# Optimization experiments

Measured on AMD Instinct MI355X. Metric: run time of the kernel, lower is better.

The kernel has to match this reference:

```python
import jax, jax.numpy as jnp
import numpy as np

B, T, D, H = 8, 1024, 512, 8
D4 = 4 * D
SIGMA = 16.0
EPS = 1e-5


def layer_norm(x, w, b):
    m = jnp.mean(x, axis=-1, keepdims=True)
    v = jnp.mean((x - m) ** 2, axis=-1, keepdims=True)
    return (x - m) * jax.lax.rsqrt(v + EPS) * w + b


def setup_inputs() -> dict:
    key = jax.random.key(0)
    ks = jax.random.split(key, 12)
    return {
        "x": jax.random.normal(ks[0], (B, T, D), jnp.float32),
        "posv": jax.random.randint(ks[1], (B, T), 0, 64, jnp.int32),
        "posh": jax.random.randint(ks[2], (B, T), 0, 64, jnp.int32),
        "norm1_w": jnp.ones((D,), jnp.float32),
        "norm1_b": jnp.zeros((D,), jnp.float32),
        "in_w": jax.random.normal(ks[3], (3 * D, D), jnp.float32) * (D ** -0.5),
        "in_b": jnp.zeros((3 * D,), jnp.float32),
        "out_w": jax.random.normal(ks[4], (D, D), jnp.float32) * (D ** -0.5),
        "out_b": jnp.zeros((D,), jnp.float32),
        "norm2_w": jnp.ones((D,), jnp.float32),
        "norm2_b": jnp.zeros((D,), jnp.float32),
        "w1": jax.random.normal(ks[5], (D4, D), jnp.float32) * (D ** -0.5),
        "b1": jnp.zeros((D4,), jnp.float32),
        "w2": jax.random.normal(ks[6], (D, D4), jnp.float32) * (D4 ** -0.5),
        "b2": jnp.zeros((D,), jnp.float32),
        "gate": jnp.array(0.0, jnp.float32),
    }


def reference(x, posv, posh, norm1_w, norm1_b, in_w, in_b, out_w, out_b,
              norm2_w, norm2_b, w1, b1, w2, b2, gate):
    hd = D // H
    residual = x
    xn = layer_norm(x, norm1_w, norm1_b)

    # --- standard multi-head self-attention (dropout=eval identity) ---
    qkv = xn @ in_w.T + in_b                       # [B,T,3D]
    q, k, v = jnp.split(qkv, 3, axis=-1)
    q = q.reshape(B, T, H, hd).transpose(0, 2, 1, 3)  # [B,H,T,hd]
    k = k.reshape(B, T, H, hd).transpose(0, 2, 1, 3)
    v = v.reshape(B, T, H, hd).transpose(0, 2, 1, 3)
    scores = jnp.einsum("bhqd,bhkd->bhqk", q, k) * (hd ** -0.5)
    attn = jax.nn.softmax(scores, axis=-1)
    ctx = jnp.einsum("bhqk,bhkd->bhqd", attn, v)   # [B,H,T,hd]
    ctx = ctx.transpose(0, 2, 1, 3).reshape(B, T, D)
    std_out = ctx @ out_w.T + out_b

    # --- Gaussian kernel position attention ---
    pos = jnp.stack([posv, posh], axis=-1).astype(jnp.float32)  # [B,T,2]
    dist_sq = jnp.sum((pos[:, :, None, :] - pos[:, None, :, :]) ** 2, axis=-1)  # [B,T,T]
    kw = jnp.exp(-dist_sq / (2.0 * SIGMA ** 2))
    kw = kw / jnp.sum(kw, axis=-1, keepdims=True)
    kernel_out = kw @ xn                            # [B,T,D]

    g = jax.nn.sigmoid(gate)
    x1 = residual + g * std_out + (1.0 - g) * kernel_out

    # --- MLP block ---
    xn2 = layer_norm(x1, norm2_w, norm2_b)
    h = jax.nn.gelu(xn2 @ w1.T + b1, approximate=False)
    return x1 + h @ w2.T + b2
```

## Files before the change

### kernel.cpp

```cpp
#include <hip/hip_runtime.h>
#include <hip/hip_bf16.h>
#include <math.h>

typedef unsigned short ushort_t;
typedef short short8 __attribute__((ext_vector_type(8)));
typedef float f32x4 __attribute__((ext_vector_type(4)));

__device__ __forceinline__ float b2f(ushort_t u) {
  union { unsigned u; float f; } v; v.u = ((unsigned)u) << 16; return v.f;
}
__device__ __forceinline__ ushort_t f2b(float f) {
  union { float f; unsigned u; } v; v.f = f;
  unsigned r = (v.u + 0x7FFFu + ((v.u >> 16) & 1u)) >> 16;
  return (ushort_t)r;
}
__device__ __forceinline__ float gelu_fast(float v) {
  float u = 0.7978845608f * (v + 0.044715f * v * v * v);
  float a = fabsf(u);
  float t = exp2f(a * -2.8853900817779268f);
  float th = (1.f - t) / (1.f + t);
  th = copysignf(th, u);
  return 0.5f * v * (1.f + th);
}

union U16x8 { uint4 v; ushort_t s[8]; };

typedef const __attribute__((address_space(1))) unsigned int glb_u32;
typedef __attribute__((address_space(3))) unsigned int lds_u32;
__device__ __forceinline__ void gl_lds16(const ushort_t* g, ushort_t* l) {
  __builtin_amdgcn_global_load_lds((glb_u32*)g, (lds_u32*)l, 16, 0, 0);
}

__global__ __launch_bounds__(256) void cvt4_kernel(const float* __restrict__ s0,
                                                   const float* __restrict__ s1,
                                                   const float* __restrict__ s2,
                                                   const float* __restrict__ s3,
                                                   ushort_t* __restrict__ d0,
                                                   ushort_t* __restrict__ d1,
                                                   ushort_t* __restrict__ d2,
                                                   ushort_t* __restrict__ d3) {
  long i = (long)blockIdx.x * 256 + threadIdx.x;
  const float* s; ushort_t* d; long off;
  if (i < 196608)       { s = s0; d = d0; off = i; }
  else if (i < 262144)  { s = s1; d = d1; off = i - 196608; }
  else if (i < 524288)  { s = s2; d = d2; off = i - 262144; }
  else                  { s = s3; d = d3; off = i - 524288; }
  float4 f = *(const float4*)(s + off * 4);
  union { uint2 v; ushort_t s[4]; } o;
  o.s[0] = f2b(f.x); o.s[1] = f2b(f.y); o.s[2] = f2b(f.z); o.s[3] = f2b(f.w);
  *(uint2*)(d + off * 4) = o.v;
}

__global__ __launch_bounds__(256) void ln_kernel(const float* __restrict__ x,
                                                 const float* __restrict__ w,
                                                 const float* __restrict__ b,
                                                 ushort_t* __restrict__ out) {
  int tid = threadIdx.x, wave = tid >> 6, lane = tid & 63;
  long token = (long)blockIdx.x * 4 + wave;
  const float* xr = x + token * 512 + lane * 8;
  float4 a0 = *(const float4*)xr;
  float4 a1 = *(const float4*)(xr + 4);
  float xf[8] = {a0.x, a0.y, a0.z, a0.w, a1.x, a1.y, a1.z, a1.w};
  float s = 0.f, sq = 0.f;
#pragma unroll
  for (int i = 0; i < 8; i++) { s += xf[i]; sq += xf[i] * xf[i]; }
#pragma unroll
  for (int off = 1; off < 64; off <<= 1) { s += __shfl_xor(s, off); sq += __shfl_xor(sq, off); }
  float m = s * (1.f / 512.f);
  float var = sq * (1.f / 512.f) - m * m;
  float rs = rsqrtf(var + 1e-5f);
  float4 w0 = *(const float4*)(w + lane * 8);
  float4 w1v = *(const float4*)(w + lane * 8 + 4);
  float4 b0 = *(const float4*)(b + lane * 8);
  float4 b1v = *(const float4*)(b + lane * 8 + 4);
  float wf[8] = {w0.x, w0.y, w0.z, w0.w, w1v.x, w1v.y, w1v.z, w1v.w};
  float bf[8] = {b0.x, b0.y, b0.z, b0.w, b1v.x, b1v.y, b1v.z, b1v.w};
  U16x8 o;
#pragma unroll
  for (int i = 0; i < 8; i++) o.s[i] = f2b((xf[i] - m) * rs * wf[i] + bf[i]);
  *(uint4*)(out + token * 512 + lane * 8) = o.v;
}

__global__ __launch_bounds__(256) void ln_b_kernel(const ushort_t* __restrict__ x,
                                                   const float* __restrict__ w,
                                                   const float* __restrict__ b,
                                                   ushort_t* __restrict__ out) {
  int tid = threadIdx.x, wave = tid >> 6, lane = tid & 63;
  long token = (long)blockIdx.x * 4 + wave;
  U16x8 ux; ux.v = *(const uint4*)(x + token * 512 + lane * 8);
  float xf[8], s = 0.f, sq = 0.f;
#pragma unroll
  for (int i = 0; i < 8; i++) { xf[i] = b2f(ux.s[i]); s += xf[i]; sq += xf[i] * xf[i]; }
#pragma unroll
  for (int off = 1; off < 64; off <<= 1) { s += __shfl_xor(s, off); sq += __shfl_xor(sq, off); }
  float m = s * (1.f / 512.f);
  float var = sq * (1.f / 512.f) - m * m;
  float rs = rsqrtf(var + 1e-5f);
  float4 w0 = *(const float4*)(w + lane * 8);
  float4 w1v = *(const float4*)(w + lane * 8 + 4);
  float4 b0 = *(const float4*)(b + lane * 8);
  float4 b1v = *(const float4*)(b + lane * 8 + 4);
  float wf[8] = {w0.x, w0.y, w0.z, w0.w, w1v.x, w1v.y, w1v.z, w1v.w};
  float bf[8] = {b0.x, b0.y, b0.z, b0.w, b1v.x, b1v.y, b1v.z, b1v.w};
  U16x8 o;
#pragma unroll
  for (int i = 0; i < 8; i++) o.s[i] = f2b((xf[i] - m) * rs * wf[i] + bf[i]);
  *(uint4*)(out + token * 512 + lane * 8) = o.v;
}

__global__ __launch_bounds__(256) void kw_kernel(const int* __restrict__ posv,
                                                 const int* __restrict__ posh,
                                                 ushort_t* __restrict__ kw) {
  int b = blockIdx.x >> 10, i = blockIdx.x & 1023;
  int tid = threadIdx.x;
  const int* pv = posv + b * 1024;
  const int* ph = posh + b * 1024;
  int pvi = pv[i], phi = ph[i];
  int j0 = tid * 4;
  int4 vj = *(const int4*)(pv + j0);
  int4 hj = *(const int4*)(ph + j0);
  int vv[4] = {vj.x, vj.y, vj.z, vj.w};
  int hh[4] = {hj.x, hj.y, hj.z, hj.w};
  float e[4]; float loc = 0.f;
#pragma unroll
  for (int u = 0; u < 4; u++) {
    int dv = pvi - vv[u], dh = phi - hh[u];
    e[u] = expf((float)(dv * dv + dh * dh) * (-1.f / 512.f));
    loc += e[u];
  }
#pragma unroll
  for (int off = 1; off < 64; off <<= 1) loc += __shfl_xor(loc, off);
  __shared__ float wsum[4];
  __shared__ float tot;
  if ((tid & 63) == 0) wsum[tid >> 6] = loc;
  __syncthreads();
  if (tid == 0) tot = wsum[0] + wsum[1] + wsum[2] + wsum[3];
  __syncthreads();
  float inv = 1.f / tot;
  union { uint2 v; ushort_t s[4]; } o;
#pragma unroll
  for (int u = 0; u < 4; u++) o.s[u] = f2b(e[u] * inv);
  *(uint2*)&kw[((long)(b * 1024 + i)) * 1024 + j0] = o.v;
}

__global__ __launch_bounds__(256) void tr_kernel(const ushort_t* __restrict__ in,
                                                 ushort_t* __restrict__ out,
                                                 int R, int C) {
  __shared__ ushort_t tile[64 * 64];
  int z = blockIdx.z, r0 = blockIdx.y * 64, c0 = blockIdx.x * 64;
  const ushort_t* src = in + (long)z * R * C;
  ushort_t* dst = out + (long)z * R * C;
  int tid = threadIdx.x;
  int tr = tid >> 2;
  const ushort_t* s = src + (long)(r0 + tr) * C + c0;
  int g = (tr + (tr >> 4)) & 7;
#pragma unroll
  for (int u = 0; u < 2; u++) {
    int c = (tid & 3) + u * 4;
    *(uint4*)&tile[tr * 64 + (c ^ g) * 8] = *(const uint4*)(s + c * 8);
  }
  __syncthreads();
  int oc = tid >> 2, ob = (tid & 3) * 16;
  U16x8 o0, o1;
#pragma unroll
  for (int j = 0; j < 16; j++) {
    int r = ob + j;
    int gg = (r + (r >> 4)) & 7;
    ushort_t val = tile[r * 64 + (((oc >> 3) ^ gg)) * 8 + (oc & 7)];
    if (j < 8) o0.s[j] = val; else o1.s[j - 8] = val;
  }
  ushort_t* d = dst + (long)(c0 + oc) * R + r0 + ob;
  *(uint4*)d = o0.v;
  *(uint4*)(d + 8) = o1.v;
}

struct GemmP {
  const ushort_t* A; const ushort_t* Bm;
  long sA, sB, sC;
  int lda, ldb, ldc, K;
  const float* biasf;
  const float* residf;
  const ushort_t* auxb;
  const float* auxf;
  float* outf;
  ushort_t* outb;
  ushort_t* qp; ushort_t* kp; ushort_t* vp;
  const float* gate;
};

template <int BM, int BN, int EPI>
__global__ __launch_bounds__(256) void gemm_k(GemmP p) {
  constexpr int TI = BM / 32, TJ = BN / 32;
  constexpr int RA = BM / 64, RB = BN / 64;
  __shared__ ushort_t As[4][BM * 32];
  __shared__ ushort_t Bs[4][BN * 32];
  int tid = threadIdx.x, wv = tid >> 6, lane = tid & 63;
  int quad = lane >> 4, l15 = lane & 15;
  int bl = blockIdx.x + gridDim.x * blockIdx.y;
  int m0 = (bl % gridDim.y) * BM;
  int n0 = (bl / gridDim.y) * BN;
  int z = blockIdx.z;
  const ushort_t* A = p.A + (long)z * p.sA;
  const ushort_t* Bm = p.Bm + (long)z * p.sB;
  int wm = (wv & 1) * (BM / 2), wn = (wv >> 1) * (BN / 2);
  f32x4 acc[TI][TJ];
#pragma unroll
  for (int i = 0; i < TI; i++)
#pragma unroll
    for (int j = 0; j < TJ; j++)
#pragma unroll
      for (int r = 0; r < 4; r++) acc[i][j][r] = 0.f;

  int srow = tid >> 2;
  int sc = ((tid & 3) ^ ((tid >> 3) & 3)) * 8;
  const ushort_t* ga = A + (long)(m0 + srow) * p.lda + sc;
  const ushort_t* gb = Bm + (long)(n0 + srow) * p.ldb + sc;
  long a64 = (long)64 * p.lda, b64 = (long)64 * p.ldb;
  int aswz = (quad ^ ((l15 >> 1) & 3)) * 8;
  int nsteps = p.K >> 5;

#pragma unroll
  for (int s = 0; s < 2; s++) {
#pragma unroll
    for (int rr = 0; rr < RA; rr++)
      gl_lds16(ga + s * 32 + rr * a64, As[s] + rr * 2048 + wv * 512);
#pragma unroll
    for (int rr = 0; rr < RB; rr++)
      gl_lds16(gb + s * 32 + rr * b64, Bs[s] + rr * 2048 + wv * 512);
  }

  for (int ks = 0; ks < nsteps; ks += 2) {
    asm volatile("s_waitcnt vmcnt(0)" ::: "memory");
    __builtin_amdgcn_s_barrier();
    if (ks + 2 < nsteps) {
#pragma unroll
      for (int s = 0; s < 2; s++) {
        int st = ks + 2 + s, bf = st & 3;
        const ushort_t* a0 = ga + st * 32;
        const ushort_t* b0 = gb + st * 32;
#pragma unroll
        for (int rr = 0; rr < RA; rr++)
          gl_lds16(a0 + rr * a64, As[bf] + rr * 2048 + wv * 512);
#pragma unroll
        for (int rr = 0; rr < RB; rr++)
          gl_lds16(b0 + rr * b64, Bs[bf] + rr * 2048 + wv * 512);
      }
    }
#pragma unroll
    for (int hs = 0; hs < 2; hs++) {
      int cur = (ks + hs) & 3;
      short8 av[TI], bv[TJ];
#pragma unroll
      for (int ti = 0; ti < TI; ti++)
        av[ti] = *(const short8*)&As[cur][(wm + ti * 16 + l15) * 32 + aswz];
#pragma unroll
      for (int tj = 0; tj < TJ; tj++)
        bv[tj] = *(const short8*)&Bs[cur][(wn + tj * 16 + l15) * 32 + aswz];
#pragma unroll
      for (int ti = 0; ti < TI; ti++)
#pragma unroll
        for (int tj = 0; tj < TJ; tj++)
          acc[ti][tj] = __builtin_amdgcn_mfma_f32_16x16x32_bf16(av[ti], bv[tj], acc[ti][tj], 0, 0, 0);
    }
  }

  float g = 0.f;
  if constexpr (EPI == 2) g = 1.f / (1.f + expf(-p.gate[0]));
#pragma unroll
  for (int ti = 0; ti < TI; ti++) {
#pragma unroll
    for (int tj = 0; tj < TJ; tj++) {
#pragma unroll
      for (int r = 0; r < 4; r++) {
        int gm = m0 + wm + ti * 16 + quad * 4 + r;
        int n = n0 + wn + tj * 16 + l15;
        float v = acc[ti][tj][r];
        if constexpr (EPI == 0) {
          v += p.biasf[n];
          int bb = gm >> 10, tt = gm & 1023;
          if (n < 512) {
            int h = n >> 6, d = n & 63;
            p.qp[((long)(bb * 8 + h) * 1024 + tt) * 64 + d] = f2b(v * 0.18033688011112042f);
          } else if (n < 1024) {
            int n2 = n - 512, h = n2 >> 6, d = n2 & 63;
            p.kp[((long)(bb * 8 + h) * 1024 + tt) * 64 + d] = f2b(v);
          } else {
            int n2 = n - 1024, h = n2 >> 6, d = n2 & 63;
            p.vp[((long)(bb * 8 + h) * 1024 + tt) * 64 + d] = f2b(v);
          }
        } else if constexpr (EPI == 1) {
          p.outb[(long)z * p.sC + (long)gm * p.ldc + n] = f2b(v);
        } else if constexpr (EPI == 2) {
          v += p.biasf[n];
          long idx = (long)gm * 512 + n;
          p.outb[idx] = f2b(p.residf[idx] + g * v + (1.f - g) * b2f(p.auxb[idx]));
        } else if constexpr (EPI == 3) {
          v += p.biasf[n];
          p.outb[(long)gm * p.ldc + n] = f2b(gelu_fast(v));
        } else {
          v += p.biasf[n];
          long idx = (long)gm * 512 + n;
          p.outf[idx] = v + b2f(p.auxb[idx]);
        }
      }
    }
  }
}

__global__ __launch_bounds__(256) void flash_k(const ushort_t* __restrict__ q,
                                               const ushort_t* __restrict__ k,
                                               const ushort_t* __restrict__ vT,
                                               ushort_t* __restrict__ ctx) {
  int bl = blockIdx.x + gridDim.x * blockIdx.y;
  int bh = bl % 64;
  int q0 = (bl / 64) * 128;
  int tid = threadIdx.x, wv = tid >> 6, lane = tid & 63;
  int quad = lane >> 4, l15 = lane & 15;
  __shared__ ushort_t Ks[2][64 * 64], Vt[2][64 * 64];
  __shared__ ushort_t Pt[128 * 64];
  int wm = wv * 32;

  short8 qf[2][2];
#pragma unroll
  for (int tq = 0; tq < 2; tq++)
#pragma unroll
    for (int kk = 0; kk < 2; kk++)
      qf[tq][kk] = *(const short8*)&q[((long)bh * 1024 + q0 + wm + tq * 16 + l15) * 64 + kk * 32 + quad * 8];

  int srow = tid >> 3;
  int sc = ((tid & 7) ^ ((tid >> 3) & 7)) * 8;
#pragma unroll
  for (int e = 0; e < 2; e++) {
    gl_lds16(&k[((long)bh * 1024 + e * 32 + srow) * 64 + sc], Ks[0] + e * 2048 + wv * 512);
    gl_lds16(&vT[((long)bh * 64 + e * 32 + srow) * 1024 + sc], Vt[0] + e * 2048 + wv * 512);
  }

  f32x4 O[2][4];
#pragma unroll
  for (int tq = 0; tq < 2; tq++)
#pragma unroll
    for (int td = 0; td < 4; td++)
#pragma unroll
      for (int r = 0; r < 4; r++) O[tq][td][r] = 0.f;
  float ls[2] = {0.f, 0.f};

  int pswz = (l15 & 7) << 1;
  for (int kt = 0; kt < 16; kt++) {
    int cur = kt & 1;
    asm volatile("s_waitcnt vmcnt(0)" ::: "memory");
    __builtin_amdgcn_s_barrier();
    if (kt + 1 < 16) {
#pragma unroll
      for (int e = 0; e < 2; e++) {
        gl_lds16(&k[((long)bh * 1024 + (kt + 1) * 64 + e * 32 + srow) * 64 + sc], Ks[cur ^ 1] + e * 2048 + wv * 512);
        gl_lds16(&vT[((long)bh * 64 + e * 32 + srow) * 1024 + (kt + 1) * 64 + sc], Vt[cur ^ 1] + e * 2048 + wv * 512);
      }
    }
#pragma unroll
    for (int tq = 0; tq < 2; tq++) {
      f32x4 S[4];
#pragma unroll
      for (int tk = 0; tk < 4; tk++) {
#pragma unroll
        for (int r = 0; r < 4; r++) S[tk][r] = 0.f;
#pragma unroll
        for (int kk = 0; kk < 2; kk++) {
          short8 kf = *(const short8*)&Ks[cur][(tk * 16 + l15) * 64 + ((kk * 4 + quad) ^ (l15 & 7)) * 8];
          S[tk] = __builtin_amdgcn_mfma_f32_16x16x32_bf16(kf, qf[tq][kk], S[tk], 0, 0, 0);
        }
      }
#pragma unroll
      for (int tk = 0; tk < 4; tk++) {
        float p0 = exp2f(S[tk][0]);
        float p1 = exp2f(S[tk][1]);
        float p2 = exp2f(S[tk][2]);
        float p3 = exp2f(S[tk][3]);
        ls[tq] += (p0 + p1) + (p2 + p3);
        unsigned lo = __builtin_amdgcn_perm(__float_as_uint(p1), __float_as_uint(p0), 0x07060302u);
        unsigned hi = __builtin_amdgcn_perm(__float_as_uint(p3), __float_as_uint(p2), 0x07060302u);
        int gnum = (tk * 4 + quad) ^ pswz;
        uint2 pr; pr.x = lo; pr.y = hi;
        *(uint2*)&Pt[(wm + tq * 16 + l15) * 64 + gnum * 4] = pr;
      }
    }
#pragma unroll
    for (int tq = 0; tq < 2; tq++) {
#pragma unroll
      for (int kk = 0; kk < 2; kk++) {
        short8 pf = *(const short8*)&Pt[(wm + tq * 16 + l15) * 64 + (((kk * 8 + quad * 2) ^ pswz)) * 4];
#pragma unroll
        for (int td = 0; td < 4; td++) {
          short8 vf = *(const short8*)&Vt[cur][(td * 16 + l15) * 64 + ((kk * 4 + quad) ^ (l15 & 7)) * 8];
          O[tq][td] = __builtin_amdgcn_mfma_f32_16x16x32_bf16(pf, vf, O[tq][td], 0, 0, 0);
        }
      }
    }
  }
#pragma unroll
  for (int tq = 0; tq < 2; tq++) {
    ls[tq] += __shfl_xor(ls[tq], 16);
    ls[tq] += __shfl_xor(ls[tq], 32);
  }
  int bb = bh >> 3, h = bh & 7;
#pragma unroll
  for (int tq = 0; tq < 2; tq++) {
#pragma unroll
    for (int r = 0; r < 4; r++) {
      int qrow = quad * 4 + r;
      float inv = 1.f / __shfl(ls[tq], (lane & 48) | qrow);
      long row = (long)bb * 1024 + q0 + wm + tq * 16 + qrow;
#pragma unroll
      for (int td = 0; td < 4; td++)
        ctx[row * 512 + h * 64 + td * 16 + l15] = f2b(O[tq][td][r] * inv);
    }
  }
}

extern "C" void kernel_launch(void* const* d_in, const int* in_sizes, int n_in,
                              void* d_out, int out_size, void* d_ws, size_t ws_size,
                              hipStream_t stream) {
  const float* x    = (const float*)d_in[0];
  const int* posv   = (const int*)d_in[1];
  const int* posh   = (const int*)d_in[2];
  const float* n1w  = (const float*)d_in[3];
  const float* n1b  = (const float*)d_in[4];
  const float* in_w = (const float*)d_in[5];
  const float* in_b = (const float*)d_in[6];
  const float* outw = (const float*)d_in[7];
  const float* outb = (const float*)d_in[8];
  const float* n2w  = (const float*)d_in[9];
  const float* n2b  = (const float*)d_in[10];
  const float* w1   = (const float*)d_in[11];
  const float* b1   = (const float*)d_in[12];
  const float* w2   = (const float*)d_in[13];
  const float* b2   = (const float*)d_in[14];
  const float* gate = (const float*)d_in[15];
  float* out = (float*)d_out;

  char* ws = (char*)d_ws;
  const size_t MB = 1024 * 1024;
  ushort_t* q    = (ushort_t*)(ws + 0 * MB);
  ushort_t* kk   = (ushort_t*)(ws + 8 * MB);
  ushort_t* vtmp = (ushort_t*)(ws + 16 * MB);
  ushort_t* vT   = (ushort_t*)(ws + 24 * MB);
  ushort_t* kw   = (ushort_t*)(ws + 32 * MB);
  ushort_t* xn   = (ushort_t*)(ws + 48 * MB);
  ushort_t* xnT  = (ushort_t*)(ws + 56 * MB);
  ushort_t* ctx  = (ushort_t*)(ws + 64 * MB);
  ushort_t* ko   = (ushort_t*)(ws + 72 * MB);
  ushort_t* x1b  = (ushort_t*)(ws + 80 * MB);
  ushort_t* xn2  = (ushort_t*)(ws + 16 * MB);
  ushort_t* inwb = (ushort_t*)(ws + 96 * MB);
  ushort_t* owb  = (ushort_t*)(ws + 98 * MB);
  ushort_t* w1b  = (ushort_t*)(ws + 99 * MB);
  ushort_t* w2b  = (ushort_t*)(ws + 101 * MB);
  ushort_t* h    = (ushort_t*)(ws + 24 * MB);

  cvt4_kernel<<<3072, 256, 0, stream>>>(in_w, outw, w1, w2, inwb, owb, w1b, w2b);
  ln_kernel<<<2048, 256, 0, stream>>>(x, n1w, n1b, xn);
  kw_kernel<<<8192, 256, 0, stream>>>(posv, posh, kw);
  {
    GemmP p = {};
    p.A = xn; p.Bm = inwb; p.lda = 512; p.ldb = 512; p.K = 512;
    p.biasf = in_b; p.qp = q; p.kp = kk; p.vp = vtmp;
    gemm_k<64, 128, 0><<<dim3(12, 128, 1), 256, 0, stream>>>(p);
  }
  tr_kernel<<<dim3(1, 16, 64), 256, 0, stream>>>(vtmp, vT, 1024, 64);
  flash_k<<<dim3(8, 64, 1), 256, 0, stream>>>(q, kk, vT, ctx);
  tr_kernel<<<dim3(8, 16, 8), 256, 0, stream>>>(xn, xnT, 1024, 512);
  {
    GemmP p = {};
    p.A = kw; p.Bm = xnT; p.lda = 1024; p.ldb = 1024; p.ldc = 512; p.K = 1024;
    p.sA = 1024L * 1024; p.sB = 512L * 1024; p.sC = 1024L * 512;
    p.outb = ko;
    gemm_k<64, 128, 1><<<dim3(4, 16, 8), 256, 0, stream>>>(p);
  }
  {
    GemmP p = {};
    p.A = ctx; p.Bm = owb; p.lda = 512; p.ldb = 512; p.K = 512;
    p.biasf = outb; p.residf = x; p.auxb = ko; p.outb = x1b; p.gate = gate;
    gemm_k<64, 64, 2><<<dim3(8, 128, 1), 256, 0, stream>>>(p);
  }
  ln_b_kernel<<<2048, 256, 0, stream>>>(x1b, n2w, n2b, xn2);
  {
    GemmP p = {};
    p.A = xn2; p.Bm = w1b; p.lda = 512; p.ldb = 512; p.ldc = 2048; p.K = 512;
    p.biasf = b1; p.outb = h;
    gemm_k<64, 128, 3><<<dim3(16, 128, 1), 256, 0, stream>>>(p);
  }
  {
    GemmP p = {};
    p.A = h; p.Bm = w2b; p.lda = 2048; p.ldb = 2048; p.K = 2048;
    p.biasf = b2; p.auxb = x1b; p.outf = out;
    gemm_k<64, 128, 4><<<dim3(4, 128, 1), 256, 0, stream>>>(p);
  }
}
```

Measured before the change: 288.2 us.

## Merge prep kernels and add per-wave independent GEMM for QKV and MLP1

Merges the weight conversion, first LayerNorm and Gaussian kernel-weight kernels into one prep launch that branches on block index. Adds a new GEMM kernel, templated on compile-time strides and K, in which each wave owns a private 64x64 output tile with its own LDS buffers. Its direct-to-LDS loads are issued without block barriers, aiming to drop the cost of __syncthreads. This kernel replaces the generic GEMM for the QKV projection and the first MLP layer. The trade-off is that waves in a block no longer share A tiles through LDS, which raises global and L2 traffic, and the LDS staging is single-buffered per wave.

```diff
diff --git a/kernel.cpp b/kernel.cpp
--- a/kernel.cpp
+++ b/kernel.cpp
@@ -31,39 +31,103 @@
   __builtin_amdgcn_global_load_lds((glb_u32*)g, (lds_u32*)l, 16, 0, 0);
 }
 
-__global__ __launch_bounds__(256) void cvt4_kernel(const float* __restrict__ s0,
+__global__ __launch_bounds__(256) void prep_kernel(const float* __restrict__ s0,
                                                    const float* __restrict__ s1,
                                                    const float* __restrict__ s2,
                                                    const float* __restrict__ s3,
                                                    ushort_t* __restrict__ d0,
                                                    ushort_t* __restrict__ d1,
                                                    ushort_t* __restrict__ d2,
-                                                   ushort_t* __restrict__ d3) {
-  long i = (long)blockIdx.x * 256 + threadIdx.x;
-  const float* s; ushort_t* d; long off;
-  if (i < 196608)       { s = s0; d = d0; off = i; }
-  else if (i < 262144)  { s = s1; d = d1; off = i - 196608; }
-  else if (i < 524288)  { s = s2; d = d2; off = i - 262144; }
-  else                  { s = s3; d = d3; off = i - 524288; }
-  float4 f = *(const float4*)(s + off * 4);
-  union { uint2 v; ushort_t s[4]; } o;
-  o.s[0] = f2b(f.x); o.s[1] = f2b(f.y); o.s[2] = f2b(f.z); o.s[3] = f2b(f.w);
-  *(uint2*)(d + off * 4) = o.v;
-}
-
-__global__ __launch_bounds__(256) void ln_kernel(const float* __restrict__ x,
-                                                 const float* __restrict__ w,
-                                                 const float* __restrict__ b,
-                                                 ushort_t* __restrict__ out) {
+                                                   ushort_t* __restrict__ d3,
+                                                   const float* __restrict__ x,
+                                                   const float* __restrict__ w,
+                                                   const float* __restrict__ b,
+                                                   ushort_t* __restrict__ xnout,
+                                                   const int* __restrict__ posv,
+                                                   const int* __restrict__ posh,
+                                                   ushort_t* __restrict__ kw) {
+  int bid = blockIdx.x;
+  int tid = threadIdx.x;
+  if (bid < 3072) {
+    long i = (long)bid * 256 + tid;
+    const float* s; ushort_t* d; long off;
+    if (i < 196608)       { s = s0; d = d0; off = i; }
+    else if (i < 262144)  { s = s1; d = d1; off = i - 196608; }
+    else if (i < 524288)  { s = s2; d = d2; off = i - 262144; }
+    else                  { s = s3; d = d3; off = i - 524288; }
+    float4 f = *(const float4*)(s + off * 4);
+    union { uint2 v; ushort_t s[4]; } o;
+    o.s[0] = f2b(f.x); o.s[1] = f2b(f.y); o.s[2] = f2b(f.z); o.s[3] = f2b(f.w);
+    *(uint2*)(d + off * 4) = o.v;
+  } else if (bid < 5120) {
+    int wave = tid >> 6, lane = tid & 63;
+    long token = (long)(bid - 3072) * 4 + wave;
+    const float* xr = x + token * 512 + lane * 8;
+    float4 a0 = *(const float4*)xr;
+    float4 a1 = *(const float4*)(xr + 4);
+    float xf[8] = {a0.x, a0.y, a0.z, a0.w, a1.x, a1.y, a1.z, a1.w};
+    float s = 0.f, sq = 0.f;
+#pragma unroll
+    for (int i = 0; i < 8; i++) { s += xf[i]; sq += xf[i] * xf[i]; }
+#pragma unroll
+    for (int off = 1; off < 64; off <<= 1) { s += __shfl_xor(s, off); sq += __shfl_xor(sq, off); }
+    float m = s * (1.f / 512.f);
+    float var = sq * (1.f / 512.f) - m * m;
+    float rs = rsqrtf(var + 1e-5f);
+    float4 w0 = *(const float4*)(w + lane * 8);
+    float4 w1v = *(const float4*)(w + lane * 8 + 4);
+    float4 b0 = *(const float4*)(b + lane * 8);
+    float4 b1v = *(const float4*)(b + lane * 8 + 4);
+    float wf[8] = {w0.x, w0.y, w0.z, w0.w, w1v.x, w1v.y, w1v.z, w1v.w};
+    float bf[8] = {b0.x, b0.y, b0.z, b0.w, b1v.x, b1v.y, b1v.z, b1v.w};
+    U16x8 o;
+#pragma unroll
+    for (int i = 0; i < 8; i++) o.s[i] = f2b((xf[i] - m) * rs * wf[i] + bf[i]);
+    *(uint4*)(xnout + token * 512 + lane * 8) = o.v;
+  } else {
+    int bb = bid - 5120;
+    int bz = bb >> 10, i = bb & 1023;
+    const int* pv = posv + bz * 1024;
+    const int* ph = posh + bz * 1024;
+    int pvi = pv[i], phi = ph[i];
+    int j0 = tid * 4;
+    int4 vj = *(const int4*)(pv + j0);
+    int4 hj = *(const int4*)(ph + j0);
+    int vv[4] = {vj.x, vj.y, vj.z, vj.w};
+    int hh[4] = {hj.x, hj.y, hj.z, hj.w};
+    float e[4]; float loc = 0.f;
+#pragma unroll
+    for (int u = 0; u < 4; u++) {
+      int dv = pvi - vv[u], dh = phi - hh[u];
+      e[u] = expf((float)(dv * dv + dh * dh) * (-1.f / 512.f));
+      loc += e[u];
+    }
+#pragma unroll
+    for (int off = 1; off < 64; off <<= 1) loc += __shfl_xor(loc, off);
+    __shared__ float wsum[4];
+    __shared__ float tot;
+    if ((tid & 63) == 0) wsum[tid >> 6] = loc;
+    __syncthreads();
+    if (tid == 0) tot = wsum[0] + wsum[1] + wsum[2] + wsum[3];
+    __syncthreads();
+    float inv = 1.f / tot;
+    union { uint2 v; ushort_t s[4]; } o;
+#pragma unroll
+    for (int u = 0; u < 4; u++) o.s[u] = f2b(e[u] * inv);
+    *(uint2*)&kw[((long)(bz * 1024 + i)) * 1024 + j0] = o.v;
+  }
+}
+
+__global__ __launch_bounds__(256) void ln_b_kernel(const ushort_t* __restrict__ x,
+                                                   const float* __restrict__ w,
+                                                   const float* __restrict__ b,
+                                                   ushort_t* __restrict__ out) {
   int tid = threadIdx.x, wave = tid >> 6, lane = tid & 63;
   long token = (long)blockIdx.x * 4 + wave;
-  const float* xr = x + token * 512 + lane * 8;
-  float4 a0 = *(const float4*)xr;
-  float4 a1 = *(const float4*)(xr + 4);
-  float xf[8] = {a0.x, a0.y, a0.z, a0.w, a1.x, a1.y, a1.z, a1.w};
-  float s = 0.f, sq = 0.f;
-#pragma unroll
-  for (int i = 0; i < 8; i++) { s += xf[i]; sq += xf[i] * xf[i]; }
+  U16x8 ux; ux.v = *(const uint4*)(x + token * 512 + lane * 8);
+  float xf[8], s = 0.f, sq = 0.f;
+#pragma unroll
+  for (int i = 0; i < 8; i++) { xf[i] = b2f(ux.s[i]); s += xf[i]; sq += xf[i] * xf[i]; }
 #pragma unroll
   for (int off = 1; off < 64; off <<= 1) { s += __shfl_xor(s, off); sq += __shfl_xor(sq, off); }
   float m = s * (1.f / 512.f);
@@ -81,68 +145,6 @@
   *(uint4*)(out + token * 512 + lane * 8) = o.v;
 }
 
-__global__ __launch_bounds__(256) void ln_b_kernel(const ushort_t* __restrict__ x,
-                                                   const float* __restrict__ w,
-                                                   const float* __restrict__ b,
-                                                   ushort_t* __restrict__ out) {
-  int tid = threadIdx.x, wave = tid >> 6, lane = tid & 63;
-  long token = (long)blockIdx.x * 4 + wave;
-  U16x8 ux; ux.v = *(const uint4*)(x + token * 512 + lane * 8);
-  float xf[8], s = 0.f, sq = 0.f;
-#pragma unroll
-  for (int i = 0; i < 8; i++) { xf[i] = b2f(ux.s[i]); s += xf[i]; sq += xf[i] * xf[i]; }
-#pragma unroll
-  for (int off = 1; off < 64; off <<= 1) { s += __shfl_xor(s, off); sq += __shfl_xor(sq, off); }
-  float m = s * (1.f / 512.f);
-  float var = sq * (1.f / 512.f) - m * m;
-  float rs = rsqrtf(var + 1e-5f);
-  float4 w0 = *(const float4*)(w + lane * 8);
-  float4 w1v = *(const float4*)(w + lane * 8 + 4);
-  float4 b0 = *(const float4*)(b + lane * 8);
-  float4 b1v = *(const float4*)(b + lane * 8 + 4);
-  float wf[8] = {w0.x, w0.y, w0.z, w0.w, w1v.x, w1v.y, w1v.z, w1v.w};
-  float bf[8] = {b0.x, b0.y, b0.z, b0.w, b1v.x, b1v.y, b1v.z, b1v.w};
-  U16x8 o;
-#pragma unroll
-  for (int i = 0; i < 8; i++) o.s[i] = f2b((xf[i] - m) * rs * wf[i] + bf[i]);
-  *(uint4*)(out + token * 512 + lane * 8) = o.v;
-}
-
-__global__ __launch_bounds__(256) void kw_kernel(const int* __restrict__ posv,
-                                                 const int* __restrict__ posh,
-                                                 ushort_t* __restrict__ kw) {
-  int b = blockIdx.x >> 10, i = blockIdx.x & 1023;
-  int tid = threadIdx.x;
-  const int* pv = posv + b * 1024;
-  const int* ph = posh + b * 1024;
-  int pvi = pv[i], phi = ph[i];
-  int j0 = tid * 4;
-  int4 vj = *(const int4*)(pv + j0);
-  int4 hj = *(const int4*)(ph + j0);
-  int vv[4] = {vj.x, vj.y, vj.z, vj.w};
-  int hh[4] = {hj.x, hj.y, hj.z, hj.w};
-  float e[4]; float loc = 0.f;
-#pragma unroll
-  for (int u = 0; u < 4; u++) {
-    int dv = pvi - vv[u], dh = phi - hh[u];
-    e[u] = expf((float)(dv * dv + dh * dh) * (-1.f / 512.f));
-    loc += e[u];
-  }
-#pragma unroll
-  for (int off = 1; off < 64; off <<= 1) loc += __shfl_xor(loc, off);
-  __shared__ float wsum[4];
-  __shared__ float tot;
-  if ((tid & 63) == 0) wsum[tid >> 6] = loc;
-  __syncthreads();
-  if (tid == 0) tot = wsum[0] + wsum[1] + wsum[2] + wsum[3];
-  __syncthreads();
-  float inv = 1.f / tot;
-  union { uint2 v; ushort_t s[4]; } o;
-#pragma unroll
-  for (int u = 0; u < 4; u++) o.s[u] = f2b(e[u] * inv);
-  *(uint2*)&kw[((long)(b * 1024 + i)) * 1024 + j0] = o.v;
-}
-
 __global__ __launch_bounds__(256) void tr_kernel(const ushort_t* __restrict__ in,
                                                  ushort_t* __restrict__ out,
                                                  int R, int C) {
@@ -181,7 +183,6 @@
   const float* biasf;
   const float* residf;
   const ushort_t* auxb;
-  const float* auxf;
   float* outf;
   ushort_t* outb;
   ushort_t* qp; ushort_t* kp; ushort_t* vp;
@@ -275,6 +276,85 @@
         int gm = m0 + wm + ti * 16 + quad * 4 + r;
         int n = n0 + wn + tj * 16 + l15;
         float v = acc[ti][tj][r];
+        if constexpr (EPI == 1) {
+          p.outb[(long)z * p.sC + (long)gm * p.ldc + n] = f2b(v);
+        } else if constexpr (EPI == 2) {
+          v += p.biasf[n];
+          long idx = (long)gm * 512 + n;
+          p.outb[idx] = f2b(p.residf[idx] + g * v + (1.f - g) * b2f(p.auxb[idx]));
+        } else {
+          v += p.biasf[n];
+          long idx = (long)gm * 512 + n;
+          p.outf[idx] = v + b2f(p.auxb[idx]);
+        }
+      }
+    }
+  }
+}
+
+template <int EPI, int LDA, int LDB, int K, int LDC>
+__global__ __launch_bounds__(256) void wgemm_k(GemmP p) {
+  constexpr int NSTEPS = K / 32;
+  constexpr long A16 = 16L * LDA, B16 = 16L * LDB;
+  __shared__ __align__(16) ushort_t lds[4][4096];
+  int tid = threadIdx.x, wv = tid >> 6, lane = tid & 63;
+  int quad = lane >> 4, l15 = lane & 15;
+  int m0 = blockIdx.x * 64;
+  int n0 = (blockIdx.y * 4 + wv) * 64;
+  ushort_t* Aw = lds[wv];
+  ushort_t* Bw = lds[wv] + 2048;
+  const ushort_t* ga = p.A + (long)(m0 + (lane >> 2)) * LDA + (lane & 3) * 8;
+  const ushort_t* gb = p.Bm + (long)(n0 + (lane >> 2)) * LDB + (lane & 3) * 8;
+
+  f32x4 acc[4][4];
+#pragma unroll
+  for (int i = 0; i < 4; i++)
+#pragma unroll
+    for (int j = 0; j < 4; j++)
+#pragma unroll
+      for (int r = 0; r < 4; r++) acc[i][j][r] = 0.f;
+
+#define WSTAGE(T)                                                \
+  {                                                              \
+    const ushort_t* a0 = ga + (T) * 32;                          \
+    const ushort_t* b0 = gb + (T) * 32;                          \
+    _Pragma("unroll")                                            \
+    for (int c = 0; c < 4; c++) gl_lds16(a0 + c * A16, Aw + c * 512); \
+    _Pragma("unroll")                                            \
+    for (int c = 0; c < 4; c++) gl_lds16(b0 + c * B16, Bw + c * 512); \
+  }
+
+  WSTAGE(0);
+  for (int t = 0; t < NSTEPS; t++) {
+    asm volatile("s_waitcnt vmcnt(0)" ::: "memory");
+    short8 av[4], bv[4];
+#pragma unroll
+    for (int i = 0; i < 4; i++) {
+      av[i] = *(const short8*)&Aw[(i * 16 + l15) * 32 + quad * 8];
+      bv[i] = *(const short8*)&Bw[(i * 16 + l15) * 32 + quad * 8];
+    }
+    asm volatile("s_waitcnt lgkmcnt(0)" ::: "memory");
+    __builtin_amdgcn_sched_barrier(0);
+    if (t + 1 < NSTEPS) WSTAGE(t + 1);
+    __builtin_amdgcn_s_setprio(1);
+#pragma unroll
+    for (int i = 0; i < 4; i++)
+#pragma unroll
+      for (int j = 0; j < 4; j++)
+        acc[i][j] = __builtin_amdgcn_mfma_f32_16x16x32_bf16(av[i], bv[j], acc[i][j], 0, 0, 0);
+    __builtin_amdgcn_s_setprio(0);
+  }
+#undef WSTAGE
+
+#pragma unroll
+  for (int ti = 0; ti < 4; ti++) {
+#pragma unroll
+    for (int tj = 0; tj < 4; tj++) {
+#pragma unroll
+      for (int r = 0; r < 4; r++) {
+        int gm = m0 + ti * 16 + quad * 4 + r;
+        int n = n0 + tj * 16 + l15;
+        float v = acc[ti][tj][r];
         if constexpr (EPI == 0) {
           v += p.biasf[n];
           int bb = gm >> 10, tt = gm & 1023;
@@ -288,19 +368,9 @@
             int n2 = n - 1024, h = n2 >> 6, d = n2 & 63;
             p.vp[((long)(bb * 8 + h) * 1024 + tt) * 64 + d] = f2b(v);
           }
-        } else if constexpr (EPI == 1) {
-          p.outb[(long)z * p.sC + (long)gm * p.ldc + n] = f2b(v);
-        } else if constexpr (EPI == 2) {
-          v += p.biasf[n];
-          long idx = (long)gm * 512 + n;
-          p.outb[idx] = f2b(p.residf[idx] + g * v + (1.f - g) * b2f(p.auxb[idx]));
-        } else if constexpr (EPI == 3) {
-          v += p.biasf[n];
-          p.outb[(long)gm * p.ldc + n] = f2b(gelu_fast(v));
         } else {
           v += p.biasf[n];
-          long idx = (long)gm * 512 + n;
-          p.outf[idx] = v + b2f(p.auxb[idx]);
+          p.outb[(long)gm * LDC + n] = f2b(gelu_fast(v));
         }
       }
     }
@@ -456,14 +526,13 @@
   ushort_t* w2b  = (ushort_t*)(ws + 101 * MB);
   ushort_t* h    = (ushort_t*)(ws + 24 * MB);
 
-  cvt4_kernel<<<3072, 256, 0, stream>>>(in_w, outw, w1, w2, inwb, owb, w1b, w2b);
-  ln_kernel<<<2048, 256, 0, stream>>>(x, n1w, n1b, xn);
-  kw_kernel<<<8192, 256, 0, stream>>>(posv, posh, kw);
+  prep_kernel<<<13312, 256, 0, stream>>>(in_w, outw, w1, w2, inwb, owb, w1b, w2b,
+                                         x, n1w, n1b, xn, posv, posh, kw);
   {
     GemmP p = {};
-    p.A = xn; p.Bm = inwb; p.lda = 512; p.ldb = 512; p.K = 512;
+    p.A = xn; p.Bm = inwb;
     p.biasf = in_b; p.qp = q; p.kp = kk; p.vp = vtmp;
-    gemm_k<64, 128, 0><<<dim3(12, 128, 1), 256, 0, stream>>>(p);
+    wgemm_k<0, 512, 512, 512, 0><<<dim3(128, 6), 256, 0, stream>>>(p);
   }
   tr_kernel<<<dim3(1, 16, 64), 256, 0, stream>>>(vtmp, vT, 1024, 64);
   flash_k<<<dim3(8, 64, 1), 256, 0, stream>>>(q, kk, vT, ctx);
@@ -484,9 +553,9 @@
   ln_b_kernel<<<2048, 256, 0, stream>>>(x1b, n2w, n2b, xn2);
   {
     GemmP p = {};
-    p.A = xn2; p.Bm = w1b; p.lda = 512; p.ldb = 512; p.ldc = 2048; p.K = 512;
+    p.A = xn2; p.Bm = w1b;
     p.biasf = b1; p.outb = h;
-    gemm_k<64, 128, 3><<<dim3(16, 128, 1), 256, 0, stream>>>(p);
+    wgemm_k<3, 512, 512, 512, 2048><<<dim3(128, 8), 256, 0, stream>>>(p);
   }
   {
     GemmP p = {};
```

Measured after the change: 290.3 us. About the same (+0.7%).
